# Performance work log

Measured on AMD Instinct MI355X. Metric: run time of the kernel, lower is better.

Reference implementation:

```python
import jax, jax.numpy as jnp
import numpy as np

D = 256      # d_model
H = 8        # n_heads
HD = D // H  # head_dim = 32
P = 16       # point dim per head


def setup_inputs() -> dict:
    key = jax.random.key(0)
    ks = jax.random.split(key, 12)
    B, S = 2, 2048
    w = lambda k, shape: jax.random.normal(k, shape, jnp.float32) * 0.02
    return {
        "seq_repr": jax.random.normal(ks[0], (B, S, D), jnp.float32),
        "coords": jax.random.normal(ks[1], (B, S, 3, 3), jnp.float32),
        "frames": jax.random.normal(ks[2], (B, S, 4), jnp.float32),
        "mask": jnp.ones((B, S), jnp.int32),
        "Wq": w(ks[3], (D, D)), "bq": jnp.zeros((D,), jnp.float32),
        "Wk": w(ks[4], (D, D)), "bk": jnp.zeros((D,), jnp.float32),
        "Wv": w(ks[5], (D, D)), "bv": jnp.zeros((D,), jnp.float32),
        "Wpq": w(ks[6], (3, H * P)), "bpq": jnp.zeros((H * P,), jnp.float32),
        "Wpk": w(ks[7], (3, H * P)), "bpk": jnp.zeros((H * P,), jnp.float32),
        "Wo": w(ks[8], (D, D)), "bo": jnp.zeros((D,), jnp.float32),
        "Wpo": w(ks[9], (H * P, 3)), "bpo": jnp.zeros((3,), jnp.float32),
        "attn_bias": jnp.zeros((H,), jnp.float32),
    }


def reference(seq_repr, coords, frames, mask, Wq, bq, Wk, bk, Wv, bv,
              Wpq, bpq, Wpk, bpk, Wo, bo, Wpo, bpo, attn_bias):
    B, S, _ = seq_repr.shape
    q = (seq_repr @ Wq + bq).reshape(B, S, H, HD)
    k = (seq_repr @ Wk + bk).reshape(B, S, H, HD)
    v = (seq_repr @ Wv + bv).reshape(B, S, H, HD)

    rep = coords[..., 1, :]                                  # [B,S,3] representative atom
    pq = (rep @ Wpq + bpq).reshape(B, S, H, P)
    pk = (rep @ Wpk + bpk).reshape(B, S, H, P)

    scale = 1.0 / np.sqrt(HD)
    scores = (jnp.einsum('bihd,bjhd->bhij', q, k) * scale
              + jnp.einsum('bihp,bjhp->bhij', pq, pk) * 0.25  # 1/sqrt(16)
              + attn_bias[None, :, None, None])

    mask2d = (mask[:, :, None] * mask[:, None, :])[:, None]  # [B,1,S,S]
    scores = jnp.where(mask2d == 0, jnp.float32(-1e9), scores)

    w = jax.nn.softmax(scores, axis=-1)                      # [B,H,S,S]

    seq_ctx = jnp.einsum('bhij,bjhd->bihd', w, v).reshape(B, S, D)
    pt_ctx = jnp.einsum('bhij,bjhp->bihp', w, pq).reshape(B, S, H * P)

    seq_out = seq_ctx @ Wo + bo                              # [B,S,D]
    point_out = pt_ctx @ Wpo + bpo                           # [B,S,3]
    return (seq_out, point_out)
```

## Files before the change

kernel.cpp:

```cpp
#include <hip/hip_runtime.h>
#include <hip/hip_bf16.h>

#define D_ 256
#define H_ 8
#define B_ 2
#define S_ 2048
#define MTOT 4096
#define AUGQ 64
#define NBH 16
#define KPAD 72
#define NJ 16

typedef __attribute__((ext_vector_type(8))) short short8;
typedef __attribute__((ext_vector_type(4))) short short4v;
typedef __attribute__((ext_vector_type(4))) float f32x4;

static __device__ __forceinline__ short bf16_of(float f) {
  union { __hip_bfloat16 h; short s; } u;
  u.h = __float2bfloat16(f);
  return u.s;
}

static __device__ __forceinline__ f32x4 mfma16(short4v a, short4v b, f32x4 c) {
#if defined(__has_builtin) && __has_builtin(__builtin_amdgcn_mfma_f32_16x16x16bf16_1k)
  return __builtin_amdgcn_mfma_f32_16x16x16bf16_1k(a, b, c, 0, 0, 0);
#else
  asm("v_mfma_f32_16x16x16_bf16 %0, %1, %2, %0" : "+v"(c) : "v"(a), "v"(b));
  return c;
#endif
}


__global__ void prep_all(const float* __restrict__ Wq, const float* __restrict__ Wk,
                         const float* __restrict__ Wv, const float* __restrict__ Wo,
                         const float* __restrict__ coords,
                         const float* __restrict__ Wpq, const float* __restrict__ bpq,
                         const float* __restrict__ Wpk, const float* __restrict__ bpk,
                         short* __restrict__ Wqkv_t, short* __restrict__ Wo_t,
                         short* __restrict__ Qa, short* __restrict__ Ka,
                         short* __restrict__ VaT) {
  int gid = blockIdx.x * 256 + threadIdx.x;
  int NT = gridDim.x * 256;
  for (int idx = gid; idx < 768 * 256; idx += NT) {
    int n = idx >> 8, k = idx & 255;
    const float* W = (n < 256) ? Wq : (n < 512 ? Wk : Wv);
    Wqkv_t[idx] = bf16_of(W[k * 256 + (n & 255)]);
  }
  for (int idx = gid; idx < 256 * 256; idx += NT) {
    int n = idx >> 8, k = idx & 255;
    Wo_t[idx] = bf16_of(Wo[k * 256 + n]);
  }
  for (int idx = gid; idx < MTOT * 128; idx += NT) {
    int m = idx >> 7, j = idx & 127;
    int h = j >> 4, p = j & 15;
    int b = m >> 11, s = m & 2047;
    float r0 = coords[m * 9 + 3], r1 = coords[m * 9 + 4], r2 = coords[m * 9 + 5];
    float pq = r0 * Wpq[j] + r1 * Wpq[128 + j] + r2 * Wpq[256 + j] + bpq[j];
    float pk = r0 * Wpk[j] + r1 * Wpk[128 + j] + r2 * Wpk[256 + j] + bpk[j];
    size_t base = ((size_t)(b * 8 + h) * S_ + s);
    Qa[base * AUGQ + 32 + p] = bf16_of(pq);
    Qa[base * AUGQ + 48 + p] = 0;
    Ka[base * AUGQ + 32 + p] = bf16_of(pk * 0.25f);
    Ka[base * AUGQ + 48 + p] = 0;
  }
  for (int idx = gid; idx < NBH * 16 * (S_ / 8); idx += NT) {
    int s8 = idx & 255, p = (idx >> 8) & 15, bh = idx >> 12;
    int b = bh >> 3, h = bh & 7, j = h * 16 + p;
    float w0 = Wpq[j], w1 = Wpq[128 + j], w2 = Wpq[256 + j], bb = bpq[j];
    short8 o;
#pragma unroll
    for (int i = 0; i < 8; i++) {
      int m = b * 2048 + s8 * 8 + i;
      o[i] = bf16_of(coords[m * 9 + 3] * w0 + coords[m * 9 + 4] * w1 +
                     coords[m * 9 + 5] * w2 + bb);
    }
    *reinterpret_cast<short8*>(&VaT[((size_t)bh * 48 + 32 + p) * S_ + s8 * 8]) = o;
  }
}


__global__ __launch_bounds__(256) void qkv_gemm(
    const float* __restrict__ X, const short* __restrict__ Wt,
    const float* __restrict__ bq, const float* __restrict__ bk, const float* __restrict__ bv,
    short* __restrict__ Qa, short* __restrict__ Ka, short* __restrict__ VaT) {
  __shared__ __align__(16) short As[64 * 136];
  __shared__ __align__(16) short Bs[64 * 136];
  int m0 = blockIdx.x * 64, n0 = blockIdx.y * 64;
  int tid = threadIdx.x, lane = tid & 63, w = tid >> 6;
  int t = lane & 15, g = lane >> 4, kf = g * 8;
  int wr = (w >> 1) * 32, wc = (w & 1) * 32;
  f32x4 acc[2][2] = {};
  int srow = tid >> 2, skc = (tid & 3) * 32;
  for (int ph = 0; ph < 2; ph++) {
    int k0 = ph * 128;
    __syncthreads();
    {
      const float* xs = &X[(size_t)(m0 + srow) * 256 + k0 + skc];
      short4v av[8];
#pragma unroll
      for (int i = 0; i < 8; i++) {
        f32x4 xv = *reinterpret_cast<const f32x4*>(&xs[i * 4]);
        short4v o;
        o[0] = bf16_of(xv[0]); o[1] = bf16_of(xv[1]);
        o[2] = bf16_of(xv[2]); o[3] = bf16_of(xv[3]);
        av[i] = o;
      }
#pragma unroll
      for (int i = 0; i < 8; i++)
        *reinterpret_cast<short4v*>(&As[srow * 136 + skc + i * 4]) = av[i];
      const uint4* wsrc = reinterpret_cast<const uint4*>(&Wt[(size_t)(n0 + srow) * 256 + k0 + skc]);
#pragma unroll
      for (int i = 0; i < 4; i++)
        *reinterpret_cast<uint4*>(&Bs[srow * 136 + skc + i * 8]) = wsrc[i];
    }
    __syncthreads();
#pragma unroll
    for (int kk = 0; kk < 4; kk++) {
      short8 a[2], bb[2];
#pragma unroll
      for (int i = 0; i < 2; i++)
        a[i] = *reinterpret_cast<const short8*>(&As[(wr + i * 16 + t) * 136 + kk * 32 + kf]);
#pragma unroll
      for (int jj = 0; jj < 2; jj++)
        bb[jj] = *reinterpret_cast<const short8*>(&Bs[(wc + jj * 16 + t) * 136 + kk * 32 + kf]);
#pragma unroll
      for (int i = 0; i < 2; i++)
#pragma unroll
        for (int jj = 0; jj < 2; jj++)
          acc[i][jj] = __builtin_amdgcn_mfma_f32_16x16x32_bf16(a[i], bb[jj], acc[i][jj], 0, 0, 0);
    }
  }
  __syncthreads();
  short* Cs = As;
  const float scale = 0.17677669529663687f;
  int b = m0 >> 11, sbase = m0 & 2047;
#pragma unroll
  for (int i = 0; i < 2; i++)
#pragma unroll
    for (int jj = 0; jj < 2; jj++)
#pragma unroll
      for (int r = 0; r < 4; r++) {
        int rl = wr + i * 16 + g * 4 + r;
        int cl = wc + jj * 16 + t;
        int n = n0 + cl;
        float v = acc[i][jj][r];
        if (n < 256) v = (v + bq[n]) * scale;
        else if (n < 512) v = v + bk[n - 256];
        else v = v + bv[n - 512];
        Cs[rl * 72 + cl] = bf16_of(v);
      }
  __syncthreads();
  if (n0 < 512) {
#pragma unroll
    for (int i2 = 0; i2 < 2; i2++) {
      int task = tid + i2 * 256;
      int row = task >> 3, c = task & 7;
      int n = n0 + c * 8;
      short* dst = (n < 256) ? Qa : Ka;
      int nn = n & 255;
      int hh = nn >> 5, d = nn & 31;
      *reinterpret_cast<short8*>(&dst[((size_t)(b * 8 + hh) * S_ + sbase + row) * AUGQ + d]) =
          *reinterpret_cast<const short8*>(&Cs[row * 72 + c * 8]);
    }
  } else {
    int hv0 = (n0 - 512) >> 5;
#pragma unroll
    for (int i2 = 0; i2 < 2; i2++) {
      int task = tid + i2 * 256;
      int fl = task >> 3, s8 = task & 7;
      short8 o;
#pragma unroll
      for (int i = 0; i < 8; i++) o[i] = Cs[(s8 * 8 + i) * 72 + fl];
      int hh = hv0 + (fl >> 5), d = fl & 31;
      *reinterpret_cast<short8*>(&VaT[((size_t)(b * 8 + hh) * 48 + d) * S_ + sbase + s8 * 8]) = o;
    }
  }
}


__global__ __launch_bounds__(256, 4) void attn(
    const short* __restrict__ Qa, const short* __restrict__ Ka,
    const short* __restrict__ VaT, const int* __restrict__ mask,
    float* __restrict__ AccO, float* __restrict__ AccL) {
  __shared__ __align__(16) char smem[32768];

  int it = blockIdx.x, h = blockIdx.y, bz = blockIdx.z;
  int b = bz >> 1, split = bz & 1;
  int tid = threadIdx.x, lane = tid & 63, w = tid >> 6;
  int t = lane & 15, g = lane >> 4, kf = g * 8;
  int q0w = it * 64 + w * 16;
  int bhv = b * H_ + h;
  size_t bh = (size_t)bhv * S_;

  short8 aq0 = *reinterpret_cast<const short8*>(&Qa[(bh + q0w + t) * AUGQ + kf]);
  short8 aq1 = *reinterpret_cast<const short8*>(&Qa[(bh + q0w + t) * AUGQ + 32 + kf]);

  f32x4 Oacc[3] = {};
  float lsum = 0.f;

  uint4 kreg0, kreg1, vreg0, vreg1;
  float mreg = 0.f;
  int srow = tid >> 3, sko = (tid & 7) * 8;
  const int jt0 = split * NJ;

  auto issue = [&](int jt) {
    const uint4* ks = reinterpret_cast<const uint4*>(&Ka[(bh + jt * 64) * AUGQ]);
    kreg0 = ks[tid];
    kreg1 = ks[tid + 256];
    size_t vb = (size_t)bhv * 48 * S_ + jt * 64;
    vreg0 = *reinterpret_cast<const uint4*>(&VaT[vb + (size_t)srow * S_ + sko]);
    if (tid < 128)
      vreg1 = *reinterpret_cast<const uint4*>(&VaT[vb + (size_t)(srow + 32) * S_ + sko]);
    if (tid < 64) mreg = mask[b * S_ + jt * 64 + tid] ? 0.f : -1e9f;
  };
  auto commit = [&](int buf) {
    short* Kd = (short*)(smem + buf * 9216);
    short* Vd = (short*)(smem + 18432 + buf * 6912);
    float* md = (float*)(smem + 32256);
    *reinterpret_cast<uint4*>(&Kd[srow * KPAD + sko]) = kreg0;
    *reinterpret_cast<uint4*>(&Kd[(srow + 32) * KPAD + sko]) = kreg1;
    *reinterpret_cast<uint4*>(&Vd[srow * KPAD + sko]) = vreg0;
    if (tid < 128)
      *reinterpret_cast<uint4*>(&Vd[(srow + 32) * KPAD + sko]) = vreg1;
    if (tid < 64) md[buf * 64 + tid] = mreg;
  };

  issue(jt0);
  commit(0);
  __syncthreads();

  for (int j = 0; j < NJ; j++) {
    int cur = j & 1;
    if (j + 1 < NJ) issue(jt0 + j + 1);
    const short* Kc = (const short*)(smem + cur * 9216);
    const short* Vc = (const short*)(smem + 18432 + cur * 6912);
    const float* mc = (const float*)(smem + 32256) + cur * 64;
    short4v pb[4];
#pragma unroll
    for (int sub = 0; sub < 4; sub++) {
      short8 ka0 = *reinterpret_cast<const short8*>(&Kc[(sub * 16 + t) * KPAD + kf]);
      short8 ka1 = *reinterpret_cast<const short8*>(&Kc[(sub * 16 + t) * KPAD + 32 + kf]);
      f32x4 s0 = {};
      s0 = __builtin_amdgcn_mfma_f32_16x16x32_bf16(ka0, aq0, s0, 0, 0, 0);
      s0 = __builtin_amdgcn_mfma_f32_16x16x32_bf16(ka1, aq1, s0, 0, 0, 0);
      f32x4 m4 = *reinterpret_cast<const f32x4*>(&mc[sub * 16 + g * 4]);
      float p0 = __expf(s0[0] + m4[0]);
      float p1 = __expf(s0[1] + m4[1]);
      float p2 = __expf(s0[2] + m4[2]);
      float p3 = __expf(s0[3] + m4[3]);
      lsum += (p0 + p1) + (p2 + p3);
      short4v pk4;
      pk4[0] = bf16_of(p0); pk4[1] = bf16_of(p1);
      pk4[2] = bf16_of(p2); pk4[3] = bf16_of(p3);
      pb[sub] = pk4;
    }
#pragma unroll
    for (int tt = 0; tt < 3; tt++) {
#pragma unroll
      for (int sub = 0; sub < 4; sub++) {
        short4v va = *reinterpret_cast<const short4v*>(&Vc[(tt * 16 + t) * KPAD + sub * 16 + g * 4]);
        Oacc[tt] = mfma16(va, pb[sub], Oacc[tt]);
      }
    }
    if (j + 1 < NJ) commit(cur ^ 1);
    __syncthreads();
  }

  lsum += __shfl_xor(lsum, 16);
  lsum += __shfl_xor(lsum, 32);

  float* Of = (float*)smem;
  size_t obase = ((size_t)(split * NBH + bhv)) * S_;
#pragma unroll
  for (int tt = 0; tt < 3; tt++)
#pragma unroll
    for (int r = 0; r < 4; r++)
      Of[(w * 16 + t) * 52 + tt * 16 + g * 4 + r] = Oacc[tt][r];
  if (lane < 16) AccL[obase + q0w + lane] = lsum;
  __syncthreads();
  int row = tid >> 2, q4 = tid & 3;
#pragma unroll
  for (int k2 = 0; k2 < 3; k2++) {
    *reinterpret_cast<f32x4*>(&AccO[(obase + it * 64 + row) * 48 + q4 * 12 + k2 * 4]) =
        *reinterpret_cast<const f32x4*>(&Of[row * 52 + q4 * 12 + k2 * 4]);
  }
}


__global__ __launch_bounds__(512) void out_gemm(
    const float* __restrict__ AccO, const float* __restrict__ AccL,
    const short* __restrict__ Wot, const float* __restrict__ bo,
    float* __restrict__ Out) {
  __shared__ __align__(16) short As[64 * 136];
  __shared__ __align__(16) short Bs[64 * 136];
  int m0 = blockIdx.x * 64, n0 = blockIdx.y * 64;
  int tid = threadIdx.x, lane = tid & 63, w = tid >> 6;
  int t = lane & 15, g = lane >> 4, kf = g * 8;
  int wm = w & 3, wn = w >> 2;
  int b = m0 >> 11, sbase = m0 & 2047;
  f32x4 acc[2] = {};
  int srow = tid >> 3, skc = (tid & 7) * 16;
  for (int ph = 0; ph < 2; ph++) {
    int k0 = ph * 128;
    __syncthreads();
    {
      int kg = k0 + skc;
      int hh = kg >> 5, d0 = kg & 31;
      size_t rowO = (size_t)(b * 8 + hh) * S_ + sbase + srow;
      float l = AccL[rowO] + AccL[rowO + (size_t)NBH * S_];
      float inv = 1.0f / l;
      size_t r0 = rowO * 48 + d0;
      size_t r1 = (rowO + (size_t)NBH * S_) * 48 + d0;
#pragma unroll
      for (int i = 0; i < 4; i++) {
        f32x4 a0 = *reinterpret_cast<const f32x4*>(&AccO[r0 + i * 4]);
        f32x4 a1 = *reinterpret_cast<const f32x4*>(&AccO[r1 + i * 4]);
        short4v o;
#pragma unroll
        for (int c = 0; c < 4; c++) o[c] = bf16_of((a0[c] + a1[c]) * inv);
        *reinterpret_cast<short4v*>(&As[srow * 136 + skc + i * 4]) = o;
      }
      *reinterpret_cast<uint4*>(&Bs[srow * 136 + skc]) =
          *reinterpret_cast<const uint4*>(&Wot[(size_t)(n0 + srow) * 256 + kg]);
      *reinterpret_cast<uint4*>(&Bs[srow * 136 + skc + 8]) =
          *reinterpret_cast<const uint4*>(&Wot[(size_t)(n0 + srow) * 256 + kg + 8]);
    }
    __syncthreads();
#pragma unroll
    for (int kk = 0; kk < 4; kk++) {
      short8 a = *reinterpret_cast<const short8*>(&As[(wm * 16 + t) * 136 + kk * 32 + kf]);
#pragma unroll
      for (int jj = 0; jj < 2; jj++) {
        short8 bb = *reinterpret_cast<const short8*>(&Bs[(wn * 32 + jj * 16 + t) * 136 + kk * 32 + kf]);
        acc[jj] = __builtin_amdgcn_mfma_f32_16x16x32_bf16(a, bb, acc[jj], 0, 0, 0);
      }
    }
  }
#pragma unroll
  for (int jj = 0; jj < 2; jj++)
#pragma unroll
    for (int r = 0; r < 4; r++) {
      int mrow = m0 + wm * 16 + g * 4 + r;
      int n = n0 + wn * 32 + jj * 16 + t;
      Out[(size_t)mrow * 256 + n] = acc[jj][r] + bo[n];
    }
}


__global__ void point_proj(const float* __restrict__ AccO, const float* __restrict__ AccL,
                           const float* __restrict__ Wpo, const float* __restrict__ bpo,
                           float* __restrict__ out) {
  int gid = blockIdx.x * 256 + threadIdx.x;
  int m = gid >> 2, qr = gid & 3;
  int b = m >> 11, s = m & 2047;
  float a0 = 0.f, a1 = 0.f, a2 = 0.f;
#pragma unroll
  for (int h2 = 0; h2 < 2; h2++) {
    int hh = qr * 2 + h2;
    size_t rowO = (size_t)(b * 8 + hh) * S_ + s;
    float inv = 1.0f / (AccL[rowO] + AccL[rowO + (size_t)NBH * S_]);
    size_t r0 = rowO * 48 + 32;
    size_t r1 = (rowO + (size_t)NBH * S_) * 48 + 32;
#pragma unroll
    for (int i = 0; i < 4; i++) {
      f32x4 v0 = *reinterpret_cast<const f32x4*>(&AccO[r0 + i * 4]);
      f32x4 v1 = *reinterpret_cast<const f32x4*>(&AccO[r1 + i * 4]);
#pragma unroll
      for (int c = 0; c < 4; c++) {
        float val = (v0[c] + v1[c]) * inv;
        int j = hh * 16 + i * 4 + c;
        a0 += val * Wpo[j * 3 + 0];
        a1 += val * Wpo[j * 3 + 1];
        a2 += val * Wpo[j * 3 + 2];
      }
    }
  }
  a0 += __shfl_xor(a0, 1); a0 += __shfl_xor(a0, 2);
  a1 += __shfl_xor(a1, 1); a1 += __shfl_xor(a1, 2);
  a2 += __shfl_xor(a2, 1); a2 += __shfl_xor(a2, 2);
  if (qr == 0) {
    out[(size_t)m * 3 + 0] = a0 + bpo[0];
    out[(size_t)m * 3 + 1] = a1 + bpo[1];
    out[(size_t)m * 3 + 2] = a2 + bpo[2];
  }
}


extern "C" void kernel_launch(void* const* d_in, const int* in_sizes, int n_in,
                              void* d_out, int out_size, void* d_ws, size_t ws_size,
                              hipStream_t stream) {
  const float* seq    = (const float*)d_in[0];
  const float* coords = (const float*)d_in[1];
  const int*   mask   = (const int*)d_in[3];
  const float* Wq  = (const float*)d_in[4];
  const float* bq  = (const float*)d_in[5];
  const float* Wk  = (const float*)d_in[6];
  const float* bk  = (const float*)d_in[7];
  const float* Wv  = (const float*)d_in[8];
  const float* bv  = (const float*)d_in[9];
  const float* Wpq = (const float*)d_in[10];
  const float* bpq = (const float*)d_in[11];
  const float* Wpk = (const float*)d_in[12];
  const float* bpk = (const float*)d_in[13];
  const float* Wo  = (const float*)d_in[14];
  const float* bo  = (const float*)d_in[15];
  const float* Wpo = (const float*)d_in[16];
  const float* bpo = (const float*)d_in[17];
  float* out = (float*)d_out;

  char* ws = (char*)d_ws;
  short* Wqkv_t = (short*)ws; ws += 768 * 256 * 2;
  short* Wo_t   = (short*)ws; ws += 256 * 256 * 2;
  short* Qa     = (short*)ws; ws += (size_t)NBH * S_ * AUGQ * 2;
  short* Ka     = (short*)ws; ws += (size_t)NBH * S_ * AUGQ * 2;
  short* VaT    = (short*)ws; ws += (size_t)NBH * 48 * S_ * 2;
  float* AccO   = (float*)ws; ws += (size_t)2 * NBH * S_ * 48 * 4;
  float* AccL   = (float*)ws; ws += (size_t)2 * NBH * S_ * 4;

  prep_all<<<1024, 256, 0, stream>>>(Wq, Wk, Wv, Wo, coords, Wpq, bpq, Wpk, bpk,
                                     Wqkv_t, Wo_t, Qa, Ka, VaT);
  qkv_gemm<<<dim3(64, 12), 256, 0, stream>>>(seq, Wqkv_t, bq, bk, bv, Qa, Ka, VaT);
  attn<<<dim3(32, 8, 4), 256, 0, stream>>>(Qa, Ka, VaT, mask, AccO, AccL);
  out_gemm<<<dim3(64, 4), 512, 0, stream>>>(AccO, AccL, Wo_t, bo, out);
  point_proj<<<64, 256, 0, stream>>>(AccO, AccL, Wpo, bpo, out + (size_t)MTOT * 256);
}
```

Before: 70.97 us.

## Fold mask into augmented QK dims, store bf16 partial context, remap attention blocks per XCD

The key mask moves into an augmented column of the Q/K operands: Q carries a constant 1 and K carries 0 or -1e9. The MFMA score therefore already includes the mask, which removes the per-tile mask load, its LDS staging and the adds in the attention loop. Split-K partial outputs are now written as bf16 instead of fp32, halving the context traffic read back by out_gemm and point_proj at some cost in precision. The attention grid becomes 1D and is remapped so blocks sharing a (batch, head, split) land on the same XCD for L2 locality. Prep writes for the point columns are also vectorised.

```diff
diff --git a/kernel.cpp b/kernel.cpp
--- a/kernel.cpp
+++ b/kernel.cpp
@@ -20,6 +20,11 @@
   u.h = __float2bfloat16(f);
   return u.s;
 }
+static __device__ __forceinline__ float f_of_bf16(short s) {
+  union { float f; unsigned int u; } u;
+  u.u = ((unsigned int)(unsigned short)s) << 16;
+  return u.f;
+}
 
 static __device__ __forceinline__ f32x4 mfma16(short4v a, short4v b, f32x4 c) {
 #if defined(__has_builtin) && __has_builtin(__builtin_amdgcn_mfma_f32_16x16x16bf16_1k)
@@ -33,7 +38,7 @@
 
 __global__ void prep_all(const float* __restrict__ Wq, const float* __restrict__ Wk,
                          const float* __restrict__ Wv, const float* __restrict__ Wo,
-                         const float* __restrict__ coords,
+                         const float* __restrict__ coords, const int* __restrict__ mask,
                          const float* __restrict__ Wpq, const float* __restrict__ bpq,
                          const float* __restrict__ Wpk, const float* __restrict__ bpk,
                          short* __restrict__ Wqkv_t, short* __restrict__ Wo_t,
@@ -50,18 +55,35 @@
     int n = idx >> 8, k = idx & 255;
     Wo_t[idx] = bf16_of(Wo[k * 256 + n]);
   }
-  for (int idx = gid; idx < MTOT * 128; idx += NT) {
-    int m = idx >> 7, j = idx & 127;
-    int h = j >> 4, p = j & 15;
+  for (int idx = gid; idx < MTOT * 8; idx += NT) {
+    int m = idx >> 3, h = idx & 7;
     int b = m >> 11, s = m & 2047;
     float r0 = coords[m * 9 + 3], r1 = coords[m * 9 + 4], r2 = coords[m * 9 + 5];
-    float pq = r0 * Wpq[j] + r1 * Wpq[128 + j] + r2 * Wpq[256 + j] + bpq[j];
-    float pk = r0 * Wpk[j] + r1 * Wpk[128 + j] + r2 * Wpk[256 + j] + bpk[j];
-    size_t base = ((size_t)(b * 8 + h) * S_ + s);
-    Qa[base * AUGQ + 32 + p] = bf16_of(pq);
-    Qa[base * AUGQ + 48 + p] = 0;
-    Ka[base * AUGQ + 32 + p] = bf16_of(pk * 0.25f);
-    Ka[base * AUGQ + 48 + p] = 0;
+    size_t base = ((size_t)(b * 8 + h) * S_ + s) * AUGQ;
+    short8 pqv[2], pkv[2];
+#pragma unroll
+    for (int c = 0; c < 2; c++)
+#pragma unroll
+      for (int i = 0; i < 8; i++) {
+        int j = h * 16 + c * 8 + i;
+        float pq = r0 * Wpq[j] + r1 * Wpq[128 + j] + r2 * Wpq[256 + j] + bpq[j];
+        float pk = r0 * Wpk[j] + r1 * Wpk[128 + j] + r2 * Wpk[256 + j] + bpk[j];
+        pqv[c][i] = bf16_of(pq);
+        pkv[c][i] = bf16_of(pk * 0.25f);
+      }
+    short8 padq = {};
+    padq[0] = 0x3F80;
+    short8 padk = {};
+    padk[0] = mask[m] ? (short)0 : bf16_of(-1e9f);
+    short8 z = {};
+    *reinterpret_cast<short8*>(&Qa[base + 32]) = pqv[0];
+    *reinterpret_cast<short8*>(&Qa[base + 40]) = pqv[1];
+    *reinterpret_cast<short8*>(&Qa[base + 48]) = padq;
+    *reinterpret_cast<short8*>(&Qa[base + 56]) = z;
+    *reinterpret_cast<short8*>(&Ka[base + 32]) = pkv[0];
+    *reinterpret_cast<short8*>(&Ka[base + 40]) = pkv[1];
+    *reinterpret_cast<short8*>(&Ka[base + 48]) = padk;
+    *reinterpret_cast<short8*>(&Ka[base + 56]) = z;
   }
   for (int idx = gid; idx < NBH * 16 * (S_ / 8); idx += NT) {
     int s8 = idx & 255, p = (idx >> 8) & 15, bh = idx >> 12;
@@ -180,16 +202,21 @@
 
 __global__ __launch_bounds__(256, 4) void attn(
     const short* __restrict__ Qa, const short* __restrict__ Ka,
-    const short* __restrict__ VaT, const int* __restrict__ mask,
-    float* __restrict__ AccO, float* __restrict__ AccL) {
-  __shared__ __align__(16) char smem[32768];
-
-  int it = blockIdx.x, h = blockIdx.y, bz = blockIdx.z;
-  int b = bz >> 1, split = bz & 1;
+    const short* __restrict__ VaT,
+    short* __restrict__ Ctx0, short* __restrict__ Ctx1,
+    float* __restrict__ AccL) {
+  __shared__ __align__(16) char smem[32256];
+
+  int bid = blockIdx.x;
+  int xcd = bid & 7, slot = bid >> 3;
+  int gidx = xcd * 4 + (slot >> 5);
+  int it = slot & 31;
+  int split = gidx & 1;
+  int bhv = gidx >> 1;
+
   int tid = threadIdx.x, lane = tid & 63, w = tid >> 6;
   int t = lane & 15, g = lane >> 4, kf = g * 8;
   int q0w = it * 64 + w * 16;
-  int bhv = b * H_ + h;
   size_t bh = (size_t)bhv * S_;
 
   short8 aq0 = *reinterpret_cast<const short8*>(&Qa[(bh + q0w + t) * AUGQ + kf]);
@@ -199,7 +226,6 @@
   float lsum = 0.f;
 
   uint4 kreg0, kreg1, vreg0, vreg1;
-  float mreg = 0.f;
   int srow = tid >> 3, sko = (tid & 7) * 8;
   const int jt0 = split * NJ;
 
@@ -211,18 +237,15 @@
     vreg0 = *reinterpret_cast<const uint4*>(&VaT[vb + (size_t)srow * S_ + sko]);
     if (tid < 128)
       vreg1 = *reinterpret_cast<const uint4*>(&VaT[vb + (size_t)(srow + 32) * S_ + sko]);
-    if (tid < 64) mreg = mask[b * S_ + jt * 64 + tid] ? 0.f : -1e9f;
   };
   auto commit = [&](int buf) {
     short* Kd = (short*)(smem + buf * 9216);
     short* Vd = (short*)(smem + 18432 + buf * 6912);
-    float* md = (float*)(smem + 32256);
     *reinterpret_cast<uint4*>(&Kd[srow * KPAD + sko]) = kreg0;
     *reinterpret_cast<uint4*>(&Kd[(srow + 32) * KPAD + sko]) = kreg1;
     *reinterpret_cast<uint4*>(&Vd[srow * KPAD + sko]) = vreg0;
     if (tid < 128)
       *reinterpret_cast<uint4*>(&Vd[(srow + 32) * KPAD + sko]) = vreg1;
-    if (tid < 64) md[buf * 64 + tid] = mreg;
   };
 
   issue(jt0);
@@ -234,7 +257,6 @@
     if (j + 1 < NJ) issue(jt0 + j + 1);
     const short* Kc = (const short*)(smem + cur * 9216);
     const short* Vc = (const short*)(smem + 18432 + cur * 6912);
-    const float* mc = (const float*)(smem + 32256) + cur * 64;
     short4v pb[4];
 #pragma unroll
     for (int sub = 0; sub < 4; sub++) {
@@ -243,11 +265,10 @@
       f32x4 s0 = {};
       s0 = __builtin_amdgcn_mfma_f32_16x16x32_bf16(ka0, aq0, s0, 0, 0, 0);
       s0 = __builtin_amdgcn_mfma_f32_16x16x32_bf16(ka1, aq1, s0, 0, 0, 0);
-      f32x4 m4 = *reinterpret_cast<const f32x4*>(&mc[sub * 16 + g * 4]);
-      float p0 = __expf(s0[0] + m4[0]);
-      float p1 = __expf(s0[1] + m4[1]);
-      float p2 = __expf(s0[2] + m4[2]);
-      float p3 = __expf(s0[3] + m4[3]);
+      float p0 = __expf(s0[0]);
+      float p1 = __expf(s0[1]);
+      float p2 = __expf(s0[2]);
+      float p3 = __expf(s0[3]);
       lsum += (p0 + p1) + (p2 + p3);
       short4v pk4;
       pk4[0] = bf16_of(p0); pk4[1] = bf16_of(p1);
@@ -270,25 +291,29 @@
   lsum += __shfl_xor(lsum, 32);
 
   float* Of = (float*)smem;
-  size_t obase = ((size_t)(split * NBH + bhv)) * S_;
 #pragma unroll
   for (int tt = 0; tt < 3; tt++)
 #pragma unroll
     for (int r = 0; r < 4; r++)
       Of[(w * 16 + t) * 52 + tt * 16 + g * 4 + r] = Oacc[tt][r];
-  if (lane < 16) AccL[obase + q0w + lane] = lsum;
+  if (lane < 16) AccL[(size_t)(split * NBH + bhv) * S_ + q0w + lane] = lsum;
   __syncthreads();
-  int row = tid >> 2, q4 = tid & 3;
-#pragma unroll
-  for (int k2 = 0; k2 < 3; k2++) {
-    *reinterpret_cast<f32x4*>(&AccO[(obase + it * 64 + row) * 48 + q4 * 12 + k2 * 4]) =
-        *reinterpret_cast<const f32x4*>(&Of[row * 52 + q4 * 12 + k2 * 4]);
+  short* CtxP = split ? Ctx1 : Ctx0;
+  size_t obase = bh + it * 64;
+  for (int task = tid; task < 384; task += 256) {
+    int row = task / 6, c8 = task % 6;
+    const float* src = &Of[row * 52 + c8 * 8];
+    short8 o;
+#pragma unroll
+    for (int i = 0; i < 8; i++) o[i] = bf16_of(src[i]);
+    *reinterpret_cast<short8*>(&CtxP[(obase + row) * 48 + c8 * 8]) = o;
   }
 }
 
 
 __global__ __launch_bounds__(512) void out_gemm(
-    const float* __restrict__ AccO, const float* __restrict__ AccL,
+    const short* __restrict__ Ctx0, const short* __restrict__ Ctx1,
+    const float* __restrict__ AccL,
     const short* __restrict__ Wot, const float* __restrict__ bo,
     float* __restrict__ Out) {
   __shared__ __align__(16) short As[64 * 136];
@@ -307,18 +332,17 @@
       int kg = k0 + skc;
       int hh = kg >> 5, d0 = kg & 31;
       size_t rowO = (size_t)(b * 8 + hh) * S_ + sbase + srow;
-      float l = AccL[rowO] + AccL[rowO + (size_t)NBH * S_];
-      float inv = 1.0f / l;
-      size_t r0 = rowO * 48 + d0;
-      size_t r1 = (rowO + (size_t)NBH * S_) * 48 + d0;
-#pragma unroll
-      for (int i = 0; i < 4; i++) {
-        f32x4 a0 = *reinterpret_cast<const f32x4*>(&AccO[r0 + i * 4]);
-        f32x4 a1 = *reinterpret_cast<const f32x4*>(&AccO[r1 + i * 4]);
-        short4v o;
-#pragma unroll
-        for (int c = 0; c < 4; c++) o[c] = bf16_of((a0[c] + a1[c]) * inv);
-        *reinterpret_cast<short4v*>(&As[srow * 136 + skc + i * 4]) = o;
+      float inv = 1.0f / (AccL[rowO] + AccL[rowO + (size_t)NBH * S_]);
+      const short8* c0 = reinterpret_cast<const short8*>(&Ctx0[rowO * 48 + d0]);
+      const short8* c1 = reinterpret_cast<const short8*>(&Ctx1[rowO * 48 + d0]);
+#pragma unroll
+      for (int half = 0; half < 2; half++) {
+        short8 a0 = c0[half], a1 = c1[half];
+        short8 o;
+#pragma unroll
+        for (int c = 0; c < 8; c++)
+          o[c] = bf16_of((f_of_bf16(a0[c]) + f_of_bf16(a1[c])) * inv);
+        *reinterpret_cast<short8*>(&As[srow * 136 + skc + half * 8]) = o;
       }
       *reinterpret_cast<uint4*>(&Bs[srow * 136 + skc]) =
           *reinterpret_cast<const uint4*>(&Wot[(size_t)(n0 + srow) * 256 + kg]);
@@ -347,7 +371,8 @@
 }
 
 
-__global__ void point_proj(const float* __restrict__ AccO, const float* __restrict__ AccL,
+__global__ void point_proj(const short* __restrict__ Ctx0, const short* __restrict__ Ctx1,
+                           const float* __restrict__ AccL,
                            const float* __restrict__ Wpo, const float* __restrict__ bpo,
                            float* __restrict__ out) {
   int gid = blockIdx.x * 256 + threadIdx.x;
@@ -359,16 +384,15 @@
     int hh = qr * 2 + h2;
     size_t rowO = (size_t)(b * 8 + hh) * S_ + s;
     float inv = 1.0f / (AccL[rowO] + AccL[rowO + (size_t)NBH * S_]);
-    size_t r0 = rowO * 48 + 32;
-    size_t r1 = (rowO + (size_t)NBH * S_) * 48 + 32;
-#pragma unroll
-    for (int i = 0; i < 4; i++) {
-      f32x4 v0 = *reinterpret_cast<const f32x4*>(&AccO[r0 + i * 4]);
-      f32x4 v1 = *reinterpret_cast<const f32x4*>(&AccO[r1 + i * 4]);
-#pragma unroll
-      for (int c = 0; c < 4; c++) {
-        float val = (v0[c] + v1[c]) * inv;
-        int j = hh * 16 + i * 4 + c;
+    const short8* c0 = reinterpret_cast<const short8*>(&Ctx0[rowO * 48 + 32]);
+    const short8* c1 = reinterpret_cast<const short8*>(&Ctx1[rowO * 48 + 32]);
+#pragma unroll
+    for (int half = 0; half < 2; half++) {
+      short8 v0 = c0[half], v1 = c1[half];
+#pragma unroll
+      for (int c = 0; c < 8; c++) {
+        float val = (f_of_bf16(v0[c]) + f_of_bf16(v1[c])) * inv;
+        int j = hh * 16 + half * 8 + c;
         a0 += val * Wpo[j * 3 + 0];
         a1 += val * Wpo[j * 3 + 1];
         a2 += val * Wpo[j * 3 + 2];
@@ -414,13 +438,14 @@
   short* Qa     = (short*)ws; ws += (size_t)NBH * S_ * AUGQ * 2;
   short* Ka     = (short*)ws; ws += (size_t)NBH * S_ * AUGQ * 2;
   short* VaT    = (short*)ws; ws += (size_t)NBH * 48 * S_ * 2;
-  float* AccO   = (float*)ws; ws += (size_t)2 * NBH * S_ * 48 * 4;
+  short* Ctx0   = (short*)ws; ws += (size_t)NBH * S_ * 48 * 2;
+  short* Ctx1   = (short*)ws; ws += (size_t)NBH * S_ * 48 * 2;
   float* AccL   = (float*)ws; ws += (size_t)2 * NBH * S_ * 4;
 
-  prep_all<<<1024, 256, 0, stream>>>(Wq, Wk, Wv, Wo, coords, Wpq, bpq, Wpk, bpk,
+  prep_all<<<1024, 256, 0, stream>>>(Wq, Wk, Wv, Wo, coords, mask, Wpq, bpq, Wpk, bpk,
                                      Wqkv_t, Wo_t, Qa, Ka, VaT);
   qkv_gemm<<<dim3(64, 12), 256, 0, stream>>>(seq, Wqkv_t, bq, bk, bv, Qa, Ka, VaT);
-  attn<<<dim3(32, 8, 4), 256, 0, stream>>>(Qa, Ka, VaT, mask, AccO, AccL);
-  out_gemm<<<dim3(64, 4), 512, 0, stream>>>(AccO, AccL, Wo_t, bo, out);
-  point_proj<<<64, 256, 0, stream>>>(AccO, AccL, Wpo, bpo, out + (size_t)MTOT * 256);
-}
+  attn<<<1024, 256, 0, stream>>>(Qa, Ka, VaT, Ctx0, Ctx1, AccL);
+  out_gemm<<<dim3(64, 4), 512, 0, stream>>>(Ctx0, Ctx1, AccL, Wo_t, bo, out);
+  point_proj<<<64, 256, 0, stream>>>(Ctx0, Ctx1, AccL, Wpo, bpo, out + (size_t)MTOT * 256);
+}
```

New measurement: 69.38 us. 1.02x faster.
